# Kernel tuning notes

Hardware: AMD Instinct MI355X
Metric: run time of the kernel (lower is better)

## Reference

```python
import jax, jax.numpy as jnp
import numpy as np

D_MODEL = 1024
N_HEADS = 16
D_HEAD = D_MODEL // N_HEADS
EPS = 1e-5


def setup_inputs() -> dict:
    key = jax.random.key(0)
    ks = jax.random.split(key, 7)
    B, T = 4, 2048
    s = 1.0 / np.sqrt(D_MODEL)
    return {
        "x": jax.random.normal(ks[0], (B, T, D_MODEL), dtype=jnp.float32),
        "ln_g": jnp.ones((D_MODEL,), jnp.float32),
        "ln_b": jnp.zeros((D_MODEL,), jnp.float32),
        "W_qkv": jax.random.normal(ks[1], (D_MODEL, 3 * D_MODEL), jnp.float32) * s,
        "b_qkv": jnp.zeros((3 * D_MODEL,), jnp.float32),
        "W_gate": jax.random.normal(ks[2], (D_MODEL, D_MODEL), jnp.float32) * s,
        "b_gate": jnp.zeros((D_MODEL,), jnp.float32),
        "W_proj": jax.random.normal(ks[3], (D_MODEL, D_MODEL), jnp.float32) * s,
        "b_proj": jnp.zeros((D_MODEL,), jnp.float32),
    }


def _forward(x, ln_g, ln_b, W_qkv, b_qkv, W_gate, b_gate, W_proj, b_proj):
    B, T, D = x.shape
    H, d = N_HEADS, D_HEAD
    # LayerNorm (eps=1e-5, biased variance as in torch)
    mu = jnp.mean(x, axis=-1, keepdims=True)
    var = jnp.mean((x - mu) ** 2, axis=-1, keepdims=True)
    x_norm = (x - mu) * jax.lax.rsqrt(var + EPS) * ln_g + ln_b
    qkv = x_norm @ W_qkv + b_qkv
    q, k, v = jnp.split(qkv, 3, axis=-1)  # each [B,T,D]
    # concept gate uses raw x
    gate = jax.nn.sigmoid(x @ W_gate + b_gate)
    gate = gate / (jnp.mean(gate, axis=-1, keepdims=True) + EPS)
    q = (q * gate).reshape(B, T, H, d)
    k = (k * gate).reshape(B, T, H, d)
    v = v.reshape(B, T, H, d)
    # ReLU^2 feature map in fp32
    q = jax.nn.relu(q.astype(jnp.float32)) ** 2 + EPS
    k = jax.nn.relu(k.astype(jnp.float32)) ** 2 + EPS
    v = v.astype(jnp.float32)
    # causal linear attention via kv recurrence (scan over T, T-major)
    qT = jnp.transpose(q, (1, 0, 2, 3))  # [T,B,H,d]
    kT = jnp.transpose(k, (1, 0, 2, 3))
    vT = jnp.transpose(v, (1, 0, 2, 3))

    def step(carry, inp):
        kv_s, k_s = carry  # [B,H,d,d], [B,H,d]
        q_t, k_t, v_t = inp  # [B,H,d]
        kv_s = kv_s + k_t[..., :, None] * v_t[..., None, :]
        k_s = k_s + k_t
        num = jnp.einsum('bhd,bhdm->bhm', q_t, kv_s)
        den = jnp.einsum('bhd,bhd->bh', q_t, k_s)[..., None] + EPS
        return (kv_s, k_s), num / den

    init = (jnp.zeros((B, H, d, d), jnp.float32), jnp.zeros((B, H, d), jnp.float32))
    _, outT = jax.lax.scan(step, init, (qT, kT, vT))  # [T,B,H,d]
    out = jnp.transpose(outT, (1, 0, 2, 3)).astype(x.dtype).reshape(B, T, D)
    return out @ W_proj + b_proj


def reference(x, ln_g, ln_b, W_qkv, b_qkv, W_gate, b_gate, W_proj, b_proj):
    return _forward(x, ln_g, ln_b, W_qkv, b_qkv, W_gate, b_gate, W_proj, b_proj)
```

## Files before the change

### kernel.cpp

```cpp
#include <hip/hip_runtime.h>
#include <math.h>

#define TOK 8192
#define DM 1024
#define EPSF 1e-5f

typedef __attribute__((ext_vector_type(8))) short short8;
typedef __attribute__((ext_vector_type(4))) float f32x4;

static __device__ __forceinline__ ushort f2bf(float f) {
  unsigned u = __float_as_uint(f);
  unsigned r = (u + 0x7fffu + ((u >> 16) & 1u)) >> 16;
  return (ushort)r;
}
static __device__ __forceinline__ float bf2f(ushort u) {
  return __uint_as_float((unsigned)u << 16);
}

static __device__ __forceinline__ void gload_lds16(const ushort* g, ushort* l) {
  __builtin_amdgcn_global_load_lds((const __attribute__((address_space(1))) void*)g,
                                   (__attribute__((address_space(3))) void*)l, 16, 0, 0);
}

static __device__ __forceinline__ int cswz(int row) {
  return (((row & 7) ^ ((row >> 3) & 7)) << 3);
}

__global__ __launch_bounds__(256) void lncvt_k(const float* __restrict__ x,
                                               const float* __restrict__ g,
                                               const float* __restrict__ b,
                                               ushort* __restrict__ x_b,
                                               ushort* __restrict__ xn_b) {
  __shared__ float red[8];
  int row = blockIdx.x;
  const float4* xr = (const float4*)(x + (size_t)row * DM);
  float4 v = xr[threadIdx.x];
  ushort4 xb4;
  xb4.x = f2bf(v.x); xb4.y = f2bf(v.y); xb4.z = f2bf(v.z); xb4.w = f2bf(v.w);
  ((ushort4*)(x_b + (size_t)row * DM))[threadIdx.x] = xb4;
  float s = v.x + v.y + v.z + v.w;
#pragma unroll
  for (int o = 32; o > 0; o >>= 1) s += __shfl_down(s, o, 64);
  int lane = threadIdx.x & 63, w = threadIdx.x >> 6;
  if (lane == 0) red[w] = s;
  __syncthreads();
  float mu = (red[0] + red[1] + red[2] + red[3]) * (1.0f / DM);
  float dx = v.x - mu, dy = v.y - mu, dz = v.z - mu, dw = v.w - mu;
  float ss = dx * dx + dy * dy + dz * dz + dw * dw;
#pragma unroll
  for (int o = 32; o > 0; o >>= 1) ss += __shfl_down(ss, o, 64);
  if (lane == 0) red[4 + w] = ss;
  __syncthreads();
  float var = (red[4] + red[5] + red[6] + red[7]) * (1.0f / DM);
  float rstd = rsqrtf(var + EPSF);
  float4 gg = ((const float4*)g)[threadIdx.x];
  float4 bb = ((const float4*)b)[threadIdx.x];
  ushort4 o4;
  o4.x = f2bf(dx * rstd * gg.x + bb.x);
  o4.y = f2bf(dy * rstd * gg.y + bb.y);
  o4.z = f2bf(dz * rstd * gg.z + bb.z);
  o4.w = f2bf(dw * rstd * gg.w + bb.w);
  ((ushort4*)(xn_b + (size_t)row * DM))[threadIdx.x] = o4;
}

__global__ __launch_bounds__(256) void tconv_k(const float* __restrict__ W,
                                               ushort* __restrict__ Wt, int K, int N) {
  __shared__ ushort tile[32][33];
  int k0 = blockIdx.y * 32, n0 = blockIdx.x * 32;
  int tx = threadIdx.x & 31, ty = threadIdx.x >> 5;
#pragma unroll
  for (int i = 0; i < 4; i++) {
    int k = ty + i * 8;
    tile[k][tx] = f2bf(W[(size_t)(k0 + k) * N + n0 + tx]);
  }
  __syncthreads();
#pragma unroll
  for (int i = 0; i < 4; i++) {
    int n = ty + i * 8;
    Wt[(size_t)(n0 + n) * K + k0 + tx] = tile[tx][n];
  }
}

__global__ __launch_bounds__(256) void gatenorm_b_k(ushort* __restrict__ gate_b) {
  __shared__ float red[4];
  int row = blockIdx.x;
  ushort4* gr = (ushort4*)(gate_b + (size_t)row * DM);
  ushort4 u4 = gr[threadIdx.x];
  float v0 = bf2f(u4.x), v1 = bf2f(u4.y), v2 = bf2f(u4.z), v3 = bf2f(u4.w);
  float s = v0 + v1 + v2 + v3;
#pragma unroll
  for (int o = 32; o > 0; o >>= 1) s += __shfl_down(s, o, 64);
  int lane = threadIdx.x & 63, w = threadIdx.x >> 6;
  if (lane == 0) red[w] = s;
  __syncthreads();
  float mean = (red[0] + red[1] + red[2] + red[3]) * (1.0f / DM);
  float inv = 1.0f / (mean + EPSF);
  u4.x = f2bf(v0 * inv); u4.y = f2bf(v1 * inv);
  u4.z = f2bf(v2 * inv); u4.w = f2bf(v3 * inv);
  gr[threadIdx.x] = u4;
}

#define BM 128
#define BN 128
#define BK 64
__global__ __launch_bounds__(256) void gemm_bf16_k(
    const ushort* __restrict__ A, const ushort* __restrict__ Bt,
    const float* __restrict__ bias, float* __restrict__ Cf,
    ushort* __restrict__ Cb, int ldc, int K, int mode) {
  __shared__ __align__(16) ushort As[BM * BK];
  __shared__ __align__(16) ushort Bs[BN * BK];
  int tid = threadIdx.x, lane = tid & 63, w = tid >> 6;
  int m0 = blockIdx.y * BM, n0 = blockIdx.x * BN;
  int wr = w >> 1, wc = w & 1;
  f32x4 acc[4][4] = {};
  for (int k0 = 0; k0 < K; k0 += BK) {
#pragma unroll
    for (int j = 0; j < 4; j++) {
      int lu = (w * 4 + j) * 64 + lane;
      int r = lu >> 3;
      int kb = (lu & 7) ^ (r & 7);
      gload_lds16(A + (size_t)(m0 + r) * K + k0 + kb * 8, &As[(w * 4 + j) * 512]);
      gload_lds16(Bt + (size_t)(n0 + r) * K + k0 + kb * 8, &Bs[(w * 4 + j) * 512]);
    }
    __syncthreads();
#pragma unroll
    for (int ks = 0; ks < 2; ks++) {
      short8 af[4], bfr[4];
      int kq = ks * 4 + (lane >> 4);
#pragma unroll
      for (int f = 0; f < 4; f++) {
        int ra = wr * 64 + f * 16 + (lane & 15);
        af[f] = *(const short8*)&As[(ra * 8 + (kq ^ (ra & 7))) * 8];
        int rb = wc * 64 + f * 16 + (lane & 15);
        bfr[f] = *(const short8*)&Bs[(rb * 8 + (kq ^ (rb & 7))) * 8];
      }
#pragma unroll
      for (int i = 0; i < 4; i++)
#pragma unroll
        for (int j2 = 0; j2 < 4; j2++)
          acc[i][j2] = __builtin_amdgcn_mfma_f32_16x16x32_bf16(af[i], bfr[j2], acc[i][j2], 0, 0, 0);
    }
    __syncthreads();
  }
#pragma unroll
  for (int i = 0; i < 4; i++) {
#pragma unroll
    for (int j2 = 0; j2 < 4; j2++) {
      int col = n0 + wc * 64 + j2 * 16 + (lane & 15);
      float bv = bias[col];
#pragma unroll
      for (int r = 0; r < 4; r++) {
        int row = m0 + wr * 64 + i * 16 + (lane >> 4) * 4 + r;
        float v = acc[i][j2][r] + bv;
        if (mode == 2) {
          v = 1.0f / (1.0f + expf(-v));
          Cb[(size_t)row * ldc + col] = f2bf(v);
        } else {
          Cf[(size_t)row * ldc + col] = v;
        }
      }
    }
  }
}

__global__ __launch_bounds__(256) void gemm_qkv_k(
    const ushort* __restrict__ A, const ushort* __restrict__ Bt,
    const float* __restrict__ bias, const ushort* __restrict__ gate_b,
    ushort* __restrict__ qb, ushort* __restrict__ kb,
    ushort* __restrict__ kt, ushort* __restrict__ vt, int K) {
  __shared__ __align__(16) ushort sh[16896];
  ushort* As = sh;
  ushort* Bs = sh + BM * BK;
  int tid = threadIdx.x, lane = tid & 63, w = tid >> 6;
  int m0 = blockIdx.y * BM, n0 = blockIdx.x * BN;
  int wr = w >> 1, wc = w & 1;
  f32x4 acc[4][4] = {};
  for (int k0 = 0; k0 < K; k0 += BK) {
#pragma unroll
    for (int j = 0; j < 4; j++) {
      int lu = (w * 4 + j) * 64 + lane;
      int r = lu >> 3;
      int kb2 = (lu & 7) ^ (r & 7);
      gload_lds16(A + (size_t)(m0 + r) * K + k0 + kb2 * 8, &As[(w * 4 + j) * 512]);
      gload_lds16(Bt + (size_t)(n0 + r) * K + k0 + kb2 * 8, &Bs[(w * 4 + j) * 512]);
    }
    __syncthreads();
#pragma unroll
    for (int ks = 0; ks < 2; ks++) {
      short8 af[4], bfr[4];
      int kq = ks * 4 + (lane >> 4);
#pragma unroll
      for (int f = 0; f < 4; f++) {
        int ra = wr * 64 + f * 16 + (lane & 15);
        af[f] = *(const short8*)&As[(ra * 8 + (kq ^ (ra & 7))) * 8];
        int rb = wc * 64 + f * 16 + (lane & 15);
        bfr[f] = *(const short8*)&Bs[(rb * 8 + (kq ^ (rb & 7))) * 8];
      }
#pragma unroll
      for (int i = 0; i < 4; i++)
#pragma unroll
        for (int j2 = 0; j2 < 4; j2++)
          acc[i][j2] = __builtin_amdgcn_mfma_f32_16x16x32_bf16(af[i], bfr[j2], acc[i][j2], 0, 0, 0);
    }
    __syncthreads();
  }
  int region = n0 >> 10;
  int n0b = n0 & 1023;
  int h0 = n0b >> 6;
  if (region < 2) {
#pragma unroll
    for (int it = 0; it < 8; it++) {
      int e = it * 256 + tid;
      int row = e >> 4, ch = e & 15;
      *(short8*)&sh[row * 132 + ch * 8] =
          *(const short8*)&gate_b[(size_t)(m0 + row) * DM + n0b + ch * 8];
    }
    __syncthreads();
#pragma unroll
    for (int i = 0; i < 4; i++) {
#pragma unroll
      for (int j2 = 0; j2 < 4; j2++) {
        int cl = wc * 64 + j2 * 16 + (lane & 15);
        float bv = bias[n0 + cl];
        int rl0 = wr * 64 + i * 16 + (lane >> 4) * 4;
#pragma unroll
        for (int r = 0; r < 4; r++) {
          float gv = bf2f(sh[(rl0 + r) * 132 + cl]);
          float v = (acc[i][j2][r] + bv) * gv;
          v = fmaxf(v, 0.0f);
          acc[i][j2][r] = v * v + EPSF;
        }
      }
    }
    __syncthreads();
  } else {
#pragma unroll
    for (int i = 0; i < 4; i++)
#pragma unroll
      for (int j2 = 0; j2 < 4; j2++) {
        int cl = wc * 64 + j2 * 16 + (lane & 15);
        float bv = bias[n0 + cl];
#pragma unroll
        for (int r = 0; r < 4; r++) acc[i][j2][r] += bv;
      }
  }
#pragma unroll
  for (int i = 0; i < 4; i++) {
#pragma unroll
    for (int j2 = 0; j2 < 4; j2++) {
      int cl = wc * 64 + j2 * 16 + (lane & 15);
      int rl0 = wr * 64 + i * 16 + (lane >> 4) * 4;
#pragma unroll
      for (int r = 0; r < 4; r++) {
        int row = rl0 + r;
        sh[row * 128 + (cl ^ cswz(row))] = f2bf(acc[i][j2][r]);
      }
    }
  }
  __syncthreads();
  if (region < 2) {
    ushort* dstRM = (region == 0) ? qb : kb;
#pragma unroll
    for (int it = 0; it < 8; it++) {
      int e = it * 256 + tid;
      int row = e >> 4, ch = e & 15;
      short8 val = *(const short8*)&sh[row * 128 + ((ch * 8) ^ cswz(row))];
      int tglob = m0 + row;
      size_t bh2 = (size_t)(tglob >> 11) * 16 + h0 + (ch >> 3);
      *(short8*)&dstRM[(bh2 * 2048 + (tglob & 2047)) * 64 + (ch & 7) * 8] = val;
    }
  }
  if (region >= 1) {
    ushort* dstT = (region == 1) ? kt : vt;
#pragma unroll
    for (int it = 0; it < 8; it++) {
      int e = it * 256 + tid;
      int tch = e & 15, dkrow = e >> 4;
      short8 val;
#pragma unroll
      for (int j = 0; j < 8; j++) {
        int row = tch * 8 + j;
        val[j] = (short)sh[row * 128 + (dkrow ^ cswz(row))];
      }
      int tglob0 = m0 + tch * 8;
      size_t bh2 = (size_t)(tglob0 >> 11) * 16 + h0 + (dkrow >> 6);
      *(short8*)&dstT[(bh2 * 64 + (dkrow & 63)) * 2048 + (tglob0 & 2047)] = val;
    }
  }
}

__global__ __launch_bounds__(256) void chunkkv_k(const ushort* __restrict__ kt,
                                                 const ushort* __restrict__ vt,
                                                 float* __restrict__ KVt,
                                                 float* __restrict__ ksum) {
  int c = blockIdx.x, bh = blockIdx.y;
  const ushort* kT = kt + (size_t)bh * 64 * 2048 + (size_t)c * 64;
  const ushort* vT = vt + (size_t)bh * 64 * 2048 + (size_t)c * 64;
  __shared__ float ksp[4][64];
  int tid = threadIdx.x, l = tid & 63, w = tid >> 6;
  int lr = l & 15, lg = l >> 4;
  f32x4 acc[4] = {};
#pragma unroll
  for (int g = 0; g < 2; g++) {
    short8 a = *(const short8*)&vT[(size_t)(w * 16 + lr) * 2048 + g * 32 + lg * 8];
#pragma unroll
    for (int n = 0; n < 4; n++) {
      short8 bk = *(const short8*)&kT[(size_t)(n * 16 + lr) * 2048 + g * 32 + lg * 8];
      acc[n] = __builtin_amdgcn_mfma_f32_16x16x32_bf16(a, bk, acc[n], 0, 0, 0);
    }
  }
  float* dst = KVt + ((size_t)bh * 32 + c) * 4096;
#pragma unroll
  for (int n = 0; n < 4; n++)
#pragma unroll
    for (int r = 0; r < 4; r++)
      dst[(w * 16 + lg * 4 + r) * 64 + n * 16 + lr] = acc[n][r];
  float s = 0.0f;
  const ushort* kr = &kT[(size_t)l * 2048 + w * 16];
#pragma unroll
  for (int j = 0; j < 16; j++) s += bf2f(kr[j]);
  ksp[w][l] = s;
  __syncthreads();
  if (tid < 64)
    ksum[((size_t)bh * 32 + c) * 64 + tid] = ksp[0][tid] + ksp[1][tid] + ksp[2][tid] + ksp[3][tid];
}

__global__ __launch_bounds__(256) void prefix_k(const float* __restrict__ KVt,
                                                ushort* __restrict__ KVb,
                                                float* __restrict__ ksum) {
  int bh = blockIdx.x;
  int gid = blockIdx.y * 256 + threadIdx.x;
  float run = 0.0f;
  if (gid < 4096) {
    for (int c2 = 0; c2 < 32; c2++) {
      size_t idx = ((size_t)bh * 32 + c2) * 4096 + gid;
      float v = KVt[idx];
      KVb[idx] = f2bf(run);
      run += v;
    }
  } else if (gid < 4160) {
    int d = gid - 4096;
    for (int c2 = 0; c2 < 32; c2++) {
      size_t idx = ((size_t)bh * 32 + c2) * 64 + d;
      float v = ksum[idx];
      ksum[idx] = run;
      run += v;
    }
  }
}

__global__ __launch_bounds__(256) void attn_k(
    const ushort* __restrict__ qb, const ushort* __restrict__ kb,
    const ushort* __restrict__ vt, const ushort* __restrict__ KVb,
    const float* __restrict__ ks, ushort* __restrict__ attnout) {
  int c = blockIdx.x, bh = blockIdx.y;
  int b = bh >> 4, h = bh & 15;
  const ushort* qB = qb + ((size_t)bh * 2048 + (size_t)c * 64) * 64;
  const ushort* kB = kb + ((size_t)bh * 2048 + (size_t)c * 64) * 64;
  const ushort* vT = vt + (size_t)bh * 64 * 2048 + (size_t)c * 64;
  const ushort* kvB = KVb + ((size_t)bh * 32 + c) * 4096;
  const float* ksP = ks + ((size_t)bh * 32 + c) * 64;
  __shared__ __align__(16) char SL[64 * 128];
  __shared__ float denp[4][64];
  __shared__ float den2p[4][64];
  __shared__ float invden[64];
  int tid = threadIdx.x, l = tid & 63, w = tid >> 6;
  int lr = l & 15, lg = l >> 4;
  {
    float d2 = 0.0f;
    const ushort* qr = &qB[(size_t)l * 64 + w * 16];
#pragma unroll
    for (int j = 0; j < 16; j++) d2 += bf2f(qr[j]) * ksP[w * 16 + j];
    den2p[w][l] = d2;
  }
#pragma unroll
  for (int n = 0; n < 4; n++) {
    f32x4 sa = {0.f, 0.f, 0.f, 0.f};
#pragma unroll
    for (int g = 0; g < 2; g++) {
      short8 a = *(const short8*)&kB[(size_t)(w * 16 + lr) * 64 + g * 32 + lg * 8];
      short8 bq = *(const short8*)&qB[(size_t)(n * 16 + lr) * 64 + g * 32 + lg * 8];
      sa = __builtin_amdgcn_mfma_f32_16x16x32_bf16(a, bq, sa, 0, 0, 0);
    }
    int t = n * 16 + lr;
    int s0 = w * 16 + lg * 4;
    float dsum = 0.0f;
    ushort sb[4];
#pragma unroll
    for (int r = 0; r < 4; r++) {
      float v = (s0 + r <= t) ? sa[r] : 0.0f;
      dsum += v;
      sb[r] = f2bf(v);
    }
    dsum += __shfl_xor(dsum, 16, 64);
    dsum += __shfl_xor(dsum, 32, 64);
    if (l < 16) denp[w][n * 16 + l] = dsum;
    int u = (s0 >> 3) ^ (t & 7);
    uint2 p;
    p.x = sb[0] | ((unsigned)sb[1] << 16);
    p.y = sb[2] | ((unsigned)sb[3] << 16);
    *(uint2*)&SL[t * 128 + u * 16 + (s0 & 7) * 2] = p;
  }
  __syncthreads();
  if (tid < 64) {
    float den = denp[0][tid] + denp[1][tid] + denp[2][tid] + denp[3][tid] +
                den2p[0][tid] + den2p[1][tid] + den2p[2][tid] + den2p[3][tid] + EPSF;
    invden[tid] = 1.0f / den;
  }
  __syncthreads();
#pragma unroll
  for (int n = 0; n < 4; n++) {
    f32x4 oa = {0.f, 0.f, 0.f, 0.f};
#pragma unroll
    for (int g = 0; g < 2; g++) {
      short8 a = *(const short8*)&kvB[(size_t)(w * 16 + lr) * 64 + g * 32 + lg * 8];
      short8 bq = *(const short8*)&qB[(size_t)(n * 16 + lr) * 64 + g * 32 + lg * 8];
      oa = __builtin_amdgcn_mfma_f32_16x16x32_bf16(a, bq, oa, 0, 0, 0);
    }
    int t = n * 16 + lr;
#pragma unroll
    for (int g = 0; g < 2; g++) {
      short8 a = *(const short8*)&vT[(size_t)(w * 16 + lr) * 2048 + g * 32 + lg * 8];
      int u = (g * 4 + lg) ^ (t & 7);
      short8 bs = *(const short8*)&SL[t * 128 + u * 16];
      oa = __builtin_amdgcn_mfma_f32_16x16x32_bf16(a, bs, oa, 0, 0, 0);
    }
    float iv = invden[t];
    ushort ob[4];
#pragma unroll
    for (int r = 0; r < 4; r++) ob[r] = f2bf(oa[r] * iv);
    size_t tok = (size_t)b * 2048 + (size_t)c * 64 + t;
    uint2 p;
    p.x = ob[0] | ((unsigned)ob[1] << 16);
    p.y = ob[2] | ((unsigned)ob[3] << 16);
    *(uint2*)&attnout[tok * 1024 + h * 64 + w * 16 + lg * 4] = p;
  }
}

extern "C" void kernel_launch(void* const* d_in, const int* in_sizes, int n_in,
                              void* d_out, int out_size, void* d_ws, size_t ws_size,
                              hipStream_t stream) {
  const float* x      = (const float*)d_in[0];
  const float* ln_g   = (const float*)d_in[1];
  const float* ln_b   = (const float*)d_in[2];
  const float* W_qkv  = (const float*)d_in[3];
  const float* b_qkv  = (const float*)d_in[4];
  const float* W_gate = (const float*)d_in[5];
  const float* b_gate = (const float*)d_in[6];
  const float* W_proj = (const float*)d_in[7];
  const float* b_proj = (const float*)d_in[8];
  float* out = (float*)d_out;

  char* wsb = (char*)d_ws;
  const size_t TD = (size_t)TOK * DM;
  const size_t SLOT = TD * 2;
  ushort* x_b     = (ushort*)(wsb + 0 * SLOT);
  ushort* attnout = (ushort*)(wsb + 0 * SLOT);
  ushort* xn_b    = (ushort*)(wsb + 1 * SLOT);
  ushort* qb      = (ushort*)(wsb + 2 * SLOT);
  ushort* kb      = (ushort*)(wsb + 3 * SLOT);
  ushort* kt      = (ushort*)(wsb + 4 * SLOT);
  ushort* vt      = (ushort*)(wsb + 5 * SLOT);
  ushort* gate_b  = (ushort*)(wsb + 6 * SLOT);
  float*  KVt     = (float*)(wsb + 6 * SLOT);
  ushort* Wt_gate = (ushort*)(wsb + 8 * SLOT);
  ushort* Wt_qkv  = (ushort*)(wsb + 8 * SLOT);
  ushort* KVb     = (ushort*)(wsb + 8 * SLOT);
  ushort* Wt_proj = (ushort*)(wsb + 9 * SLOT);
  float*  ksum    = (float*)(wsb + 9 * SLOT + 8 * 1024 * 1024);

  lncvt_k<<<TOK, 256, 0, stream>>>(x, ln_g, ln_b, x_b, xn_b);
  tconv_k<<<dim3(DM / 32, DM / 32), 256, 0, stream>>>(W_gate, Wt_gate, DM, DM);
  gemm_bf16_k<<<dim3(DM / BN, TOK / BM), 256, 0, stream>>>(x_b, Wt_gate, b_gate, nullptr,
                                                           gate_b, DM, DM, 2);
  gatenorm_b_k<<<TOK, 256, 0, stream>>>(gate_b);
  tconv_k<<<dim3(3 * DM / 32, DM / 32), 256, 0, stream>>>(W_qkv, Wt_qkv, DM, 3 * DM);
  gemm_qkv_k<<<dim3(3 * DM / BN, TOK / BM), 256, 0, stream>>>(xn_b, Wt_qkv, b_qkv, gate_b,
                                                              qb, kb, kt, vt, DM);
  chunkkv_k<<<dim3(32, 64), 256, 0, stream>>>(kt, vt, KVt, ksum);
  tconv_k<<<dim3(DM / 32, DM / 32), 256, 0, stream>>>(W_proj, Wt_proj, DM, DM);
  prefix_k<<<dim3(64, 17), 256, 0, stream>>>(KVt, KVb, ksum);
  attn_k<<<dim3(32, 64), 256, 0, stream>>>(qb, kb, vt, KVb, ksum, attnout);
  gemm_bf16_k<<<dim3(DM / BN, TOK / BM), 256, 0, stream>>>(attnout, Wt_proj, b_proj, out,
                                                           nullptr, DM, DM, 0);
}
```

Baseline: 216.5 us.

## Fuse chunk KV with prefix scan, fold gate norm into QKV, remap GEMM blocks

Replaces the in-place gate normalization kernel with a per-row inverse-mean kernel and applies that scale inside the QKV GEMM epilogue. Merges the chunk-KV and prefix-scan kernels into one kernel that keeps the running KV state in MFMA accumulators and writes the bf16 prefix directly, which removes the fp32 KVt round trip. Adds an XCD-aware block remapping to both GEMMs to improve L2 locality, and vectorizes the q loads in the attention denominator. The fused prefix kernel launches only 256 blocks and runs a serial 32-step loop, so it has much less parallelism than the kernels it replaces.

```diff
diff --git a/kernel.cpp b/kernel.cpp
--- a/kernel.cpp
+++ b/kernel.cpp
@@ -24,6 +24,14 @@
 
 static __device__ __forceinline__ int cswz(int row) {
   return (((row & 7) ^ ((row >> 3) & 7)) << 3);
+}
+
+static __device__ __forceinline__ int2 xcd_remap(int nx) {
+  int bid = blockIdx.y * nx + blockIdx.x;
+  int nwg = nx * gridDim.y;
+  int cpx = nwg >> 3;
+  int id = (bid & 7) * cpx + (bid >> 3);
+  return make_int2(id % nx, id / nx);
 }
 
 __global__ __launch_bounds__(256) void lncvt_k(const float* __restrict__ x,
@@ -81,23 +89,18 @@
   }
 }
 
-__global__ __launch_bounds__(256) void gatenorm_b_k(ushort* __restrict__ gate_b) {
-  __shared__ float red[4];
-  int row = blockIdx.x;
-  ushort4* gr = (ushort4*)(gate_b + (size_t)row * DM);
-  ushort4 u4 = gr[threadIdx.x];
-  float v0 = bf2f(u4.x), v1 = bf2f(u4.y), v2 = bf2f(u4.z), v3 = bf2f(u4.w);
-  float s = v0 + v1 + v2 + v3;
-#pragma unroll
-  for (int o = 32; o > 0; o >>= 1) s += __shfl_down(s, o, 64);
-  int lane = threadIdx.x & 63, w = threadIdx.x >> 6;
-  if (lane == 0) red[w] = s;
-  __syncthreads();
-  float mean = (red[0] + red[1] + red[2] + red[3]) * (1.0f / DM);
-  float inv = 1.0f / (mean + EPSF);
-  u4.x = f2bf(v0 * inv); u4.y = f2bf(v1 * inv);
-  u4.z = f2bf(v2 * inv); u4.w = f2bf(v3 * inv);
-  gr[threadIdx.x] = u4;
+__global__ __launch_bounds__(256) void rowinv_k(const ushort* __restrict__ gate_b,
+                                                float* __restrict__ ginv) {
+  int row = blockIdx.x * 4 + (threadIdx.x >> 6);
+  int l = threadIdx.x & 63;
+  const short8* gr = (const short8*)(gate_b + (size_t)row * DM);
+  short8 g0 = gr[l * 2], g1 = gr[l * 2 + 1];
+  float s = 0.f;
+#pragma unroll
+  for (int j = 0; j < 8; j++) s += bf2f((ushort)g0[j]) + bf2f((ushort)g1[j]);
+#pragma unroll
+  for (int o = 1; o < 64; o <<= 1) s += __shfl_xor(s, o, 64);
+  if (l == 0) ginv[row] = 1.0f / (s * (1.0f / DM) + EPSF);
 }
 
 #define BM 128
@@ -110,7 +113,8 @@
   __shared__ __align__(16) ushort As[BM * BK];
   __shared__ __align__(16) ushort Bs[BN * BK];
   int tid = threadIdx.x, lane = tid & 63, w = tid >> 6;
-  int m0 = blockIdx.y * BM, n0 = blockIdx.x * BN;
+  int2 bxy = xcd_remap(gridDim.x);
+  int m0 = bxy.y * BM, n0 = bxy.x * BN;
   int wr = w >> 1, wc = w & 1;
   f32x4 acc[4][4] = {};
   for (int k0 = 0; k0 < K; k0 += BK) {
@@ -166,13 +170,16 @@
 __global__ __launch_bounds__(256) void gemm_qkv_k(
     const ushort* __restrict__ A, const ushort* __restrict__ Bt,
     const float* __restrict__ bias, const ushort* __restrict__ gate_b,
+    const float* __restrict__ ginv,
     ushort* __restrict__ qb, ushort* __restrict__ kb,
     ushort* __restrict__ kt, ushort* __restrict__ vt, int K) {
   __shared__ __align__(16) ushort sh[16896];
+  __shared__ float ginvs[128];
   ushort* As = sh;
   ushort* Bs = sh + BM * BK;
   int tid = threadIdx.x, lane = tid & 63, w = tid >> 6;
-  int m0 = blockIdx.y * BM, n0 = blockIdx.x * BN;
+  int2 bxy = xcd_remap(gridDim.x);
+  int m0 = bxy.y * BM, n0 = bxy.x * BN;
   int wr = w >> 1, wc = w & 1;
   f32x4 acc[4][4] = {};
   for (int k0 = 0; k0 < K; k0 += BK) {
@@ -208,6 +215,7 @@
   int n0b = n0 & 1023;
   int h0 = n0b >> 6;
   if (region < 2) {
+    if (tid < 128) ginvs[tid] = ginv[m0 + tid];
 #pragma unroll
     for (int it = 0; it < 8; it++) {
       int e = it * 256 + tid;
@@ -225,7 +233,7 @@
         int rl0 = wr * 64 + i * 16 + (lane >> 4) * 4;
 #pragma unroll
         for (int r = 0; r < 4; r++) {
-          float gv = bf2f(sh[(rl0 + r) * 132 + cl]);
+          float gv = bf2f(sh[(rl0 + r) * 132 + cl]) * ginvs[rl0 + r];
           float v = (acc[i][j2][r] + bv) * gv;
           v = fmaxf(v, 0.0f);
           acc[i][j2][r] = v * v + EPSF;
@@ -289,63 +297,43 @@
   }
 }
 
-__global__ __launch_bounds__(256) void chunkkv_k(const ushort* __restrict__ kt,
-                                                 const ushort* __restrict__ vt,
-                                                 float* __restrict__ KVt,
-                                                 float* __restrict__ ksum) {
-  int c = blockIdx.x, bh = blockIdx.y;
-  const ushort* kT = kt + (size_t)bh * 64 * 2048 + (size_t)c * 64;
-  const ushort* vT = vt + (size_t)bh * 64 * 2048 + (size_t)c * 64;
-  __shared__ float ksp[4][64];
+__global__ __launch_bounds__(256) void chunkpfx_k(const ushort* __restrict__ kt,
+                                                  const ushort* __restrict__ vt,
+                                                  ushort* __restrict__ KVb,
+                                                  float* __restrict__ ksum) {
+  int dvs = blockIdx.x, bh = blockIdx.y;
   int tid = threadIdx.x, l = tid & 63, w = tid >> 6;
   int lr = l & 15, lg = l >> 4;
-  f32x4 acc[4] = {};
-#pragma unroll
-  for (int g = 0; g < 2; g++) {
-    short8 a = *(const short8*)&vT[(size_t)(w * 16 + lr) * 2048 + g * 32 + lg * 8];
-#pragma unroll
-    for (int n = 0; n < 4; n++) {
-      short8 bk = *(const short8*)&kT[(size_t)(n * 16 + lr) * 2048 + g * 32 + lg * 8];
-      acc[n] = __builtin_amdgcn_mfma_f32_16x16x32_bf16(a, bk, acc[n], 0, 0, 0);
-    }
-  }
-  float* dst = KVt + ((size_t)bh * 32 + c) * 4096;
-#pragma unroll
-  for (int n = 0; n < 4; n++)
-#pragma unroll
-    for (int r = 0; r < 4; r++)
-      dst[(w * 16 + lg * 4 + r) * 64 + n * 16 + lr] = acc[n][r];
-  float s = 0.0f;
-  const ushort* kr = &kT[(size_t)l * 2048 + w * 16];
-#pragma unroll
-  for (int j = 0; j < 16; j++) s += bf2f(kr[j]);
-  ksp[w][l] = s;
-  __syncthreads();
-  if (tid < 64)
-    ksum[((size_t)bh * 32 + c) * 64 + tid] = ksp[0][tid] + ksp[1][tid] + ksp[2][tid] + ksp[3][tid];
-}
-
-__global__ __launch_bounds__(256) void prefix_k(const float* __restrict__ KVt,
-                                                ushort* __restrict__ KVb,
-                                                float* __restrict__ ksum) {
-  int bh = blockIdx.x;
-  int gid = blockIdx.y * 256 + threadIdx.x;
-  float run = 0.0f;
-  if (gid < 4096) {
-    for (int c2 = 0; c2 < 32; c2++) {
-      size_t idx = ((size_t)bh * 32 + c2) * 4096 + gid;
-      float v = KVt[idx];
-      KVb[idx] = f2bf(run);
-      run += v;
-    }
-  } else if (gid < 4160) {
-    int d = gid - 4096;
-    for (int c2 = 0; c2 < 32; c2++) {
-      size_t idx = ((size_t)bh * 32 + c2) * 64 + d;
-      float v = ksum[idx];
-      ksum[idx] = run;
-      run += v;
-    }
+  const ushort* vT = vt + ((size_t)bh * 64 + dvs * 16 + lr) * 2048;
+  const ushort* kT = kt + ((size_t)bh * 64 + w * 16 + lr) * 2048;
+  f32x4 run = {0.f, 0.f, 0.f, 0.f};
+  float runks = 0.0f;
+  short8 a0 = *(const short8*)&vT[lg * 8];
+  short8 a1 = *(const short8*)&vT[32 + lg * 8];
+  short8 b0 = *(const short8*)&kT[lg * 8];
+  short8 b1 = *(const short8*)&kT[32 + lg * 8];
+  for (int c = 0; c < 32; c++) {
+    ushort* dst = KVb + ((size_t)bh * 32 + c) * 4096 +
+                  (size_t)(dvs * 16 + lg * 4) * 64 + w * 16 + lr;
+    dst[0] = f2bf(run[0]); dst[64] = f2bf(run[1]);
+    dst[128] = f2bf(run[2]); dst[192] = f2bf(run[3]);
+    if (dvs == 0) {
+      float s = 0.f;
+#pragma unroll
+      for (int j = 0; j < 8; j++) s += bf2f((ushort)b0[j]) + bf2f((ushort)b1[j]);
+      s += __shfl_xor(s, 16, 64);
+      s += __shfl_xor(s, 32, 64);
+      if (l < 16) ksum[((size_t)bh * 32 + c) * 64 + w * 16 + l] = runks;
+      runks += s;
+    }
+    int cn = (c + 1) & 31;
+    short8 na0 = *(const short8*)&vT[cn * 64 + lg * 8];
+    short8 na1 = *(const short8*)&vT[cn * 64 + 32 + lg * 8];
+    short8 nb0 = *(const short8*)&kT[cn * 64 + lg * 8];
+    short8 nb1 = *(const short8*)&kT[cn * 64 + 32 + lg * 8];
+    run = __builtin_amdgcn_mfma_f32_16x16x32_bf16(a0, b0, run, 0, 0, 0);
+    run = __builtin_amdgcn_mfma_f32_16x16x32_bf16(a1, b1, run, 0, 0, 0);
+    a0 = na0; a1 = na1; b0 = nb0; b1 = nb1;
   }
 }
 
@@ -367,10 +355,14 @@
   int tid = threadIdx.x, l = tid & 63, w = tid >> 6;
   int lr = l & 15, lg = l >> 4;
   {
+    short8 q0 = *(const short8*)&qB[(size_t)l * 64 + w * 16];
+    short8 q1 = *(const short8*)&qB[(size_t)l * 64 + w * 16 + 8];
     float d2 = 0.0f;
-    const ushort* qr = &qB[(size_t)l * 64 + w * 16];
-#pragma unroll
-    for (int j = 0; j < 16; j++) d2 += bf2f(qr[j]) * ksP[w * 16 + j];
+#pragma unroll
+    for (int j = 0; j < 8; j++) {
+      d2 += bf2f((ushort)q0[j]) * ksP[w * 16 + j];
+      d2 += bf2f((ushort)q1[j]) * ksP[w * 16 + 8 + j];
+    }
     den2p[w][l] = d2;
   }
 #pragma unroll
@@ -462,24 +454,23 @@
   ushort* kt      = (ushort*)(wsb + 4 * SLOT);
   ushort* vt      = (ushort*)(wsb + 5 * SLOT);
   ushort* gate_b  = (ushort*)(wsb + 6 * SLOT);
-  float*  KVt     = (float*)(wsb + 6 * SLOT);
   ushort* Wt_gate = (ushort*)(wsb + 8 * SLOT);
   ushort* Wt_qkv  = (ushort*)(wsb + 8 * SLOT);
   ushort* KVb     = (ushort*)(wsb + 8 * SLOT);
   ushort* Wt_proj = (ushort*)(wsb + 9 * SLOT);
   float*  ksum    = (float*)(wsb + 9 * SLOT + 8 * 1024 * 1024);
+  float*  ginv    = (float*)(wsb + 9 * SLOT + 12 * 1024 * 1024);
 
   lncvt_k<<<TOK, 256, 0, stream>>>(x, ln_g, ln_b, x_b, xn_b);
   tconv_k<<<dim3(DM / 32, DM / 32), 256, 0, stream>>>(W_gate, Wt_gate, DM, DM);
   gemm_bf16_k<<<dim3(DM / BN, TOK / BM), 256, 0, stream>>>(x_b, Wt_gate, b_gate, nullptr,
                                                            gate_b, DM, DM, 2);
-  gatenorm_b_k<<<TOK, 256, 0, stream>>>(gate_b);
+  rowinv_k<<<TOK / 4, 256, 0, stream>>>(gate_b, ginv);
   tconv_k<<<dim3(3 * DM / 32, DM / 32), 256, 0, stream>>>(W_qkv, Wt_qkv, DM, 3 * DM);
   gemm_qkv_k<<<dim3(3 * DM / BN, TOK / BM), 256, 0, stream>>>(xn_b, Wt_qkv, b_qkv, gate_b,
-                                                              qb, kb, kt, vt, DM);
-  chunkkv_k<<<dim3(32, 64), 256, 0, stream>>>(kt, vt, KVt, ksum);
+                                                              ginv, qb, kb, kt, vt, DM);
+  chunkpfx_k<<<dim3(4, 64), 256, 0, stream>>>(kt, vt, KVb, ksum);
   tconv_k<<<dim3(DM / 32, DM / 32), 256, 0, stream>>>(W_proj, Wt_proj, DM, DM);
-  prefix_k<<<dim3(64, 17), 256, 0, stream>>>(KVt, KVb, ksum);
   attn_k<<<dim3(32, 64), 256, 0, stream>>>(qb, kb, vt, KVb, ksum, attnout);
   gemm_bf16_k<<<dim3(DM / BN, TOK / BM), 256, 0, stream>>>(attnout, Wt_proj, b_proj, out,
                                                            nullptr, DM, DM, 0);
```

New measurement: 211.7 us. 1.02x faster.
